# Optimization experiments

Measured on AMD Instinct MI355X. Metric: run time of the kernel, lower is better.

## Reference

```python
import jax, jax.numpy as jnp
import numpy as np

EMBED = 128; HEADS = 8; LEVELS = 3; POINTS = 4
SCENE = (128, 128, 8)
IMG_H, IMG_W = 370, 1226
VOXEL_SIZE = 0.4; OFFSET = 0.5
FEAT_SHAPES = ((47, 154), (24, 77), (12, 39))  # (H, W) per level, strides ~8/16/32
NVOX = SCENE[0] * SCENE[1] * SCENE[2]
DH = EMBED // HEADS


def layernorm(x, g, b, eps=1e-5):
    mu = x.mean(-1, keepdims=True)
    var = ((x - mu) ** 2).mean(-1, keepdims=True)
    return (x - mu) * jax.lax.rsqrt(var + eps) * g + b


def ms_deform(value, locs, aw):
    # value [B,Nv,H,Dh]; locs [B,Q,H,L,P,2] normalized (x,y); aw [B,Q,H,L,P]
    # Matches F.grid_sample(bilinear, zeros padding, align_corners=False):
    # pixel = loc * size - 0.5, per-corner gather with zeroed out-of-range weights.
    B, Nv, Hh, Dh = value.shape
    Q, P = locs.shape[1], locs.shape[4]
    out = jnp.zeros((B, Hh, Q, Dh), value.dtype)
    start = 0
    for l, (h, w) in enumerate(FEAT_SHAPES):
        v = value[:, start:start + h * w].transpose(0, 2, 1, 3)  # [B,H,h*w,Dh]
        start += h * w
        x = locs[:, :, :, l, :, 0] * w - 0.5  # [B,Q,H,P]
        y = locs[:, :, :, l, :, 1] * h - 0.5
        x0, y0 = jnp.floor(x), jnp.floor(y)
        a_l = aw[:, :, :, l]  # [B,Q,H,P]
        for dx in (0, 1):
            for dy in (0, 1):
                xi, yi = x0 + dx, y0 + dy
                wgt = (1.0 - jnp.abs(x - xi)) * (1.0 - jnp.abs(y - yi))
                valid = (xi >= 0) & (xi <= w - 1) & (yi >= 0) & (yi <= h - 1)
                coef = wgt * valid * a_l  # bilinear weight * attention weight
                idx = (jnp.clip(yi, 0, h - 1) * w + jnp.clip(xi, 0, w - 1)).astype(jnp.int32)
                idx = idx.transpose(0, 2, 1, 3).reshape(B, Hh, Q * P, 1)
                g = jnp.take_along_axis(v, idx, axis=2).reshape(B, Hh, Q, P, Dh)
                out = out + jnp.einsum('bhqpd,bqhp->bhqd', g, coef)
    return out.transpose(0, 2, 1, 3).reshape(B, Q, Hh * Dh)


def _forward(scene_embed, feat0, feat1, feat2, depth, K, E, voxel_origin, ref_pix,
             W_off, b_off, W_attn, b_attn, W_val, b_val, W_out, b_out,
             ln1_g, ln1_b, W_ffn1, b_ffn1, W_ffn2, b_ffn2, ln2_g, ln2_b):
    B = scene_embed.shape[0]
    # ---- camera-to-voxel projection (builds pts_mask) ----
    u = jnp.arange(IMG_W, dtype=jnp.float32)
    v = jnp.arange(IMG_H, dtype=jnp.float32)
    grid = jnp.stack([jnp.broadcast_to(u[None, :], (IMG_H, IMG_W)),
                      jnp.broadcast_to(v[:, None], (IMG_H, IMG_W))])[None]  # [1,2,H,W] (u,v)
    d = depth[:, None]  # [B,1,H,W]
    p_x = jnp.concatenate([grid * d, d], axis=1).reshape(B, 3, -1)  # homogeneous pixels
    p_c = jnp.linalg.inv(K) @ p_x  # camera frame [B,3,N]
    ones = jnp.ones((B, 1, p_c.shape[-1]), p_c.dtype)
    p_w = jnp.linalg.inv(E) @ jnp.concatenate([p_c, ones], axis=1)  # world frame [B,4,N]
    # torch .long() truncates toward zero -> jnp.trunc
    p_v = jnp.trunc((p_w[:, :3].transpose(0, 2, 1) - voxel_origin[:, None]) / VOXEL_SIZE - OFFSET).astype(jnp.int32)
    X, Y, Z = SCENE
    keep = ((p_v[..., 0] >= 0) & (p_v[..., 0] < X) &
            (p_v[..., 1] >= 0) & (p_v[..., 1] < Y) &
            (p_v[..., 2] >= 0) & (p_v[..., 2] < Z))
    lin = (p_v[..., 0] * Y + p_v[..., 1]) * Z + p_v[..., 2]
    lin = jnp.where(keep, lin, 0)
    pts_mask = (jnp.zeros((NVOX,), jnp.int32).at[lin[0]].max(keep[0].astype(jnp.int32)) > 0)

    # ---- MSDeformAttn layer over ALL voxel queries (per-query math is independent;
    #      masked selection + scatter-back is equivalent to a final where) ----
    feat_flat = jnp.concatenate(
        [f.reshape(B, EMBED, -1).transpose(0, 2, 1) for f in (feat0, feat1, feat2)], axis=1)
    value = (feat_flat @ W_val + b_val).reshape(B, -1, HEADS, DH)
    q = scene_embed  # [B,NVOX,C]
    off = (q @ W_off + b_off).reshape(B, NVOX, HEADS, LEVELS, POINTS, 2)
    aw = jax.nn.softmax((q @ W_attn + b_attn).reshape(B, NVOX, HEADS, LEVELS * POINTS), axis=-1)
    aw = aw.reshape(B, NVOX, HEADS, LEVELS, POINTS)
    norm = jnp.array([[w, h] for (h, w) in FEAT_SHAPES], jnp.float32)  # (W,H) per level
    locs = ref_pix[:, :, None, None, None, :] + off / norm[None, None, None, :, None, :]
    sampled = ms_deform(value, locs, aw)  # [B,NVOX,C]
    x = layernorm(sampled @ W_out + b_out + q, ln1_g, ln1_b)       # attn residual + norm1
    h = jax.nn.gelu(x @ W_ffn1 + b_ffn1, approximate=False)        # exact GELU (torch default)
    x = layernorm(h @ W_ffn2 + b_ffn2 + x, ln2_g, ln2_b)           # ffn residual + norm2

    # ---- index_fov_back_to_voxels: masked voxels get attn output, rest keep input ----
    return jnp.where(pts_mask[None, :, None], x, scene_embed)


def setup_inputs() -> dict:
    key = jax.random.key(0)
    ks = jax.random.split(key, 16)
    d = {}
    d['scene_embed'] = jax.random.normal(ks[0], (1, NVOX, EMBED), jnp.float32)
    for i, (h, w) in enumerate(FEAT_SHAPES):
        d[f'feat{i}'] = jax.random.normal(ks[1 + i], (1, EMBED, h, w), jnp.float32)
    d['depth'] = jax.random.uniform(ks[4], (1, IMG_H, IMG_W), jnp.float32) * 50.0 + 2.0
    d['K'] = jnp.array([[[707.0, 0.0, 602.0], [0.0, 707.0, 183.0], [0.0, 0.0, 1.0]]], jnp.float32)
    c, s = float(np.cos(0.02)), float(np.sin(0.02))
    d['E'] = jnp.array([[[c, -s, 0.0, 0.5], [s, c, 0.0, 0.1],
                         [0.0, 0.0, 1.0, -1.6], [0.0, 0.0, 0.0, 1.0]]], jnp.float32)
    d['voxel_origin'] = jnp.array([[0.0, -25.6, -2.0]], jnp.float32)
    d['ref_pix'] = jax.random.uniform(ks[5], (1, NVOX, 2), jnp.float32)

    def lin(k, fin, fout):
        s = 1.0 / float(np.sqrt(fin))
        kw, kb = jax.random.split(k)
        return (jax.random.uniform(kw, (fin, fout), jnp.float32, -s, s),
                jax.random.uniform(kb, (fout,), jnp.float32, -s, s))

    d['W_off'], d['b_off'] = lin(ks[6], EMBED, HEADS * LEVELS * POINTS * 2)
    d['W_attn'], d['b_attn'] = lin(ks[7], EMBED, HEADS * LEVELS * POINTS)
    d['W_val'], d['b_val'] = lin(ks[8], EMBED, EMBED)
    d['W_out'], d['b_out'] = lin(ks[9], EMBED, EMBED)
    d['ln1_g'] = jnp.ones((EMBED,), jnp.float32); d['ln1_b'] = jnp.zeros((EMBED,), jnp.float32)
    d['W_ffn1'], d['b_ffn1'] = lin(ks[10], EMBED, EMBED * 4)
    d['W_ffn2'], d['b_ffn2'] = lin(ks[11], EMBED * 4, EMBED)
    d['ln2_g'] = jnp.ones((EMBED,), jnp.float32); d['ln2_b'] = jnp.zeros((EMBED,), jnp.float32)
    return d


def reference(scene_embed, feat0, feat1, feat2, depth, K, E, voxel_origin, ref_pix,
              W_off, b_off, W_attn, b_attn, W_val, b_val, W_out, b_out,
              ln1_g, ln1_b, W_ffn1, b_ffn1, W_ffn2, b_ffn2, ln2_g, ln2_b):
    return _forward(scene_embed, feat0, feat1, feat2, depth, K, E, voxel_origin, ref_pix,
                    W_off, b_off, W_attn, b_attn, W_val, b_val, W_out, b_out,
                    ln1_g, ln1_b, W_ffn1, b_ffn1, W_ffn2, b_ffn2, ln2_g, ln2_b)
```

## Files before the change

kernel.cpp:

```cpp
#include <hip/hip_runtime.h>
#include <math.h>

#define NVOXT 131072
#define NPIX  (370*1226)
#define NVAL  9554
#define DMT   16

#define OFF_INV    0
#define OFF_CNT    256
#define OFF_MASK   512
#define OFF_LIST   (512 + 4*NVOXT)
#define OFF_VALUE  (OFF_LIST + 4*NVOXT)

__device__ void gauss_inv(const float* A, double* out, int n) {
    double a[4][8];
    for (int r = 0; r < n; r++)
        for (int c = 0; c < n; c++) {
            a[r][c]     = (double)A[r*n + c];
            a[r][n + c] = (r == c) ? 1.0 : 0.0;
        }
    for (int col = 0; col < n; col++) {
        int piv = col; double best = fabs(a[col][col]);
        for (int r = col + 1; r < n; r++) {
            double m = fabs(a[r][col]);
            if (m > best) { best = m; piv = r; }
        }
        if (piv != col)
            for (int c = 0; c < 2*n; c++) { double t = a[col][c]; a[col][c] = a[piv][c]; a[piv][c] = t; }
        double dinv = 1.0 / a[col][col];
        for (int c = 0; c < 2*n; c++) a[col][c] *= dinv;
        for (int r = 0; r < n; r++) if (r != col) {
            double f = a[r][col];
            for (int c = 0; c < 2*n; c++) a[r][c] -= f * a[col][c];
        }
    }
    for (int r = 0; r < n; r++)
        for (int c = 0; c < n; c++) out[r*n + c] = a[r][n + c];
}

__global__ void zero_kernel(int* mask, int* cnt, const float* Km, const float* Em,
                            double* inv) {
    int i = blockIdx.x * 256 + threadIdx.x;
    if (i < NVOXT) mask[i] = 0;
    if (i == 0) *cnt = 0;
    if (blockIdx.x == 512) {
        if (threadIdx.x == 0) gauss_inv(Km, inv, 3);
        if (threadIdx.x == 1) gauss_inv(Em, inv + 9, 4);
    }
}

__global__ void mask_kernel(const float* depth, const float* org,
                            const double* invd, int* mask) {
    __shared__ float iK[9], iE[12];
    if (threadIdx.x < 9)  iK[threadIdx.x] = (float)invd[threadIdx.x];
    if (threadIdx.x < 12) iE[threadIdx.x] = (float)invd[9 + threadIdx.x];
    __syncthreads();
    int i = blockIdx.x * 256 + threadIdx.x;
    if (i >= NPIX) return;
    int u = i % 1226, v = i / 1226;
    float d  = depth[i];
    float px = (float)u * d, py = (float)v * d, pz = d;
    float c0 = iK[0]*px + iK[1]*py + iK[2]*pz;
    float c1 = iK[3]*px + iK[4]*py + iK[5]*pz;
    float c2 = iK[6]*px + iK[7]*py + iK[8]*pz;
    float w0 = iE[0]*c0 + iE[1]*c1 + iE[2]*c2  + iE[3];
    float w1 = iE[4]*c0 + iE[5]*c1 + iE[6]*c2  + iE[7];
    float w2 = iE[8]*c0 + iE[9]*c1 + iE[10]*c2 + iE[11];
    float q0 = truncf((w0 - org[0]) / 0.4f - 0.5f);
    float q1 = truncf((w1 - org[1]) / 0.4f - 0.5f);
    float q2 = truncf((w2 - org[2]) / 0.4f - 0.5f);
    if (q0 >= 0.0f && q0 < 128.0f && q1 >= 0.0f && q1 < 128.0f && q2 >= 0.0f && q2 < 8.0f) {
        int lin = (((int)q0) * 128 + (int)q1) * 8 + (int)q2;
        atomicOr(&mask[lin], 1);
    }
}

__global__ void compact_kernel(const int* mask, int* list, int* cnt) {
    int v = blockIdx.x * 256 + threadIdx.x;
    if (v < NVOXT && mask[v]) {
        int p = atomicAdd(cnt, 1);
        list[p] = v;
    }
}

__global__ void copy_kernel(const float4* src, float4* dst) {
    int i = blockIdx.x * 256 + threadIdx.x;
    dst[i] = src[i];
}

__global__ __launch_bounds__(128) void value_kernel(
    const float* f0, const float* f1, const float* f2,
    const float* Wv, const float* bv, float* value) {
    __shared__ __align__(16) float As[16*129];
    int n0 = blockIdx.x * 16;
    int t  = threadIdx.x;
    for (int i = 0; i < 16; i++) {
        int flat = t + i*128;
        int k = flat >> 4, r = flat & 15;
        int n = n0 + r;
        float vload = 0.f;
        if (n < NVAL) {
            const float* f; int p, hw;
            if (n < 7238)      { f = f0; p = n;        hw = 7238; }
            else if (n < 9086) { f = f1; p = n - 7238; hw = 1848; }
            else               { f = f2; p = n - 9086; hw = 468;  }
            vload = f[k*hw + p];
        }
        As[r*129 + k] = vload;
    }
    __syncthreads();
    float acc[16];
    float bb = bv[t];
    #pragma unroll
    for (int r = 0; r < 16; r++) acc[r] = bb;
    for (int k = 0; k < 128; k++) {
        float w = Wv[k*128 + t];
        #pragma unroll
        for (int r = 0; r < 16; r++) acc[r] += As[r*129 + k] * w;
    }
    for (int r = 0; r < 16; r++) {
        int n = n0 + r;
        if (n < NVAL) value[n*128 + t] = acc[r];
    }
}

#define FMA4(A, s, Vv) { A[0] += (s)*(Vv).x; A[1] += (s)*(Vv).y; A[2] += (s)*(Vv).z; A[3] += (s)*(Vv).w; }

__global__ __launch_bounds__(256) void deform_kernel(
    const float* scene, const float* refpix,
    const float* Woff, const float* Wattn,
    const float* boff, const float* battn,
    const float* value, const float* Wout, const float* bout,
    const float* ln1g, const float* ln1b,
    const int* list, const int* cntp, float* out) {
    __shared__ __align__(16) float sQ[DMT*132];
    __shared__ __align__(16) float sW[9216];
    __shared__ __align__(16) float sOA[DMT*292];
    __shared__ __align__(16) float sSamp[DMT*132];

    const int count = *cntp;
    const int r0 = blockIdx.x * DMT;
    if (r0 >= count) return;
    const int t = threadIdx.x;

    for (int i = 0; i < 8; i++) {
        int flat = t + i*256;
        int m = flat >> 7, e = flat & 127;
        int r = r0 + m;
        float qv = 0.f;
        if (r < count) qv = scene[(size_t)list[r]*128 + e];
        sQ[m*132 + e] = qv;
    }
    __syncthreads();

    const int tn = t & 31, tm = t >> 5;
    float acc[3][2][4] = {};

    for (int c = 0; c < 4; c++) {
        __syncthreads();
        for (int i = 0; i < 24; i++) {
            int flat = t + i*256;
            int kk = flat / 192, n = flat % 192;
            sW[kk*288 + n] = Woff[(c*32 + kk)*192 + n];
        }
        for (int i = 0; i < 12; i++) {
            int flat = t + i*256;
            int kk = flat / 96, na = flat % 96;
            sW[kk*288 + 192 + na] = Wattn[(c*32 + kk)*96 + na];
        }
        __syncthreads();
        for (int kk = 0; kk < 32; kk++) {
            int k = c*32 + kk;
            float a0 = sQ[(2*tm)*132 + k];
            float a1 = sQ[(2*tm+1)*132 + k];
            float4 w0 = *(const float4*)&sW[kk*288 + 4*tn];
            float4 w1 = *(const float4*)&sW[kk*288 + 128 + 4*tn];
            FMA4(acc[0][0], a0, w0); FMA4(acc[0][1], a1, w0);
            FMA4(acc[1][0], a0, w1); FMA4(acc[1][1], a1, w1);
            if (tn < 8) {
                float4 w2 = *(const float4*)&sW[kk*288 + 256 + 4*tn];
                FMA4(acc[2][0], a0, w2); FMA4(acc[2][1], a1, w2);
            }
        }
    }
    for (int p = 0; p < 3; p++) {
        if (p == 2 && tn >= 8) continue;
        int nbase = p*128 + 4*tn;
        for (int i = 0; i < 2; i++)
            for (int j = 0; j < 4; j++) {
                int n = nbase + j;
                float bias = (n < 192) ? boff[n] : battn[n - 192];
                sOA[(2*tm+i)*292 + n] = acc[p][i][j] + bias;
            }
    }
    __syncthreads();

    {
        int v = t >> 4;
        int h = (t >> 1) & 7;
        int d0 = (t & 1) * 8;
        int r = r0 + v;
        int vox = (r < count) ? list[r] : list[0];
        float rx = refpix[vox*2 + 0], ry = refpix[vox*2 + 1];

        float L[12];
        float mx = -1e30f;
        #pragma unroll
        for (int j = 0; j < 12; j++) {
            L[j] = sOA[v*292 + 192 + h*12 + j];
            mx = fmaxf(mx, L[j]);
        }
        float s = 0.f;
        #pragma unroll
        for (int j = 0; j < 12; j++) { L[j] = expf(L[j] - mx); s += L[j]; }
        float inv_s = 1.f / s;

        const int   STl[3] = {0, 7238, 9086};
        const float FWl[3] = {154.f, 77.f, 39.f};
        const float FHl[3] = {47.f, 24.f, 12.f};

        float accA[4] = {0,0,0,0}, accB[4] = {0,0,0,0};
        for (int l = 0; l < 3; l++) {
            float fw = FWl[l], fh = FHl[l];
            int   st = STl[l];
            int   iw = (int)fw;
            for (int p = 0; p < 4; p++) {
                float ox = sOA[v*292 + h*24 + l*8 + p*2 + 0];
                float oy = sOA[v*292 + h*24 + l*8 + p*2 + 1];
                float x = rx*fw + ox - 0.5f;
                float y = ry*fh + oy - 0.5f;
                float aw = L[l*4 + p] * inv_s;
                float x0 = floorf(x), y0 = floorf(y);
                #pragma unroll
                for (int dy = 0; dy <= 1; dy++)
                #pragma unroll
                for (int dx = 0; dx <= 1; dx++) {
                    float xi = x0 + dx, yi = y0 + dy;
                    if (xi >= 0.f && xi <= fw - 1.f && yi >= 0.f && yi <= fh - 1.f) {
                        float cf = (1.f - fabsf(x - xi)) * (1.f - fabsf(y - yi)) * aw;
                        int idx = (int)yi * iw + (int)xi;
                        const float* vp = value + ((size_t)(st + idx)*128 + h*16 + d0);
                        float4 va = *(const float4*)vp;
                        float4 vb = *(const float4*)(vp + 4);
                        FMA4(accA, cf, va);
                        FMA4(accB, cf, vb);
                    }
                }
            }
        }
        float* sp = &sSamp[v*132 + h*16 + d0];
        *(float4*)sp       = make_float4(accA[0], accA[1], accA[2], accA[3]);
        *(float4*)(sp + 4) = make_float4(accB[0], accB[1], accB[2], accB[3]);
    }
    __syncthreads();

    float acc2[2][4] = {};
    for (int c = 0; c < 2; c++) {
        __syncthreads();
        for (int i = 0; i < 32; i++) {
            int flat = t + i*256;
            sW[flat] = Wout[c*8192 + flat];
        }
        __syncthreads();
        for (int kk = 0; kk < 64; kk++) {
            int k = c*64 + kk;
            float a0 = sSamp[(2*tm)*132 + k];
            float a1 = sSamp[(2*tm+1)*132 + k];
            float4 w = *(const float4*)&sW[kk*128 + 4*tn];
            FMA4(acc2[0], a0, w); FMA4(acc2[1], a1, w);
        }
    }
    __syncthreads();
    float* sX = sOA;
    for (int i = 0; i < 2; i++)
        for (int j = 0; j < 4; j++) {
            int n = 4*tn + j, m = 2*tm + i;
            sX[m*132 + n] = acc2[i][j] + bout[n] + sQ[m*132 + n];
        }
    __syncthreads();

    {
        int row = t >> 4, j16 = t & 15;
        float xs[8], s1 = 0.f, s2 = 0.f;
        #pragma unroll
        for (int q = 0; q < 8; q++) {
            float xv = sX[row*132 + j16*8 + q];
            xs[q] = xv; s1 += xv; s2 += xv*xv;
        }
        #pragma unroll
        for (int off = 8; off >= 1; off >>= 1) {
            s1 += __shfl_xor(s1, off, 16);
            s2 += __shfl_xor(s2, off, 16);
        }
        float mu  = s1 * (1.f/128.f);
        float var = s2 * (1.f/128.f) - mu*mu;
        float rs  = 1.f / sqrtf(var + 1e-5f);
        int r = r0 + row;
        if (r < count) {
            int vox = list[r];
            #pragma unroll
            for (int q = 0; q < 8; q++) {
                int e = j16*8 + q;
                out[(size_t)vox*128 + e] = (xs[q] - mu) * rs * ln1g[e] + ln1b[e];
            }
        }
    }
}

__global__ __launch_bounds__(256) void ffn_kernel(
    const float* W1, const float* b1,
    const float* W2, const float* b2,
    const float* ln2g, const float* ln2b,
    const int* list, const int* cntp, float* out) {
    __shared__ __align__(16) float sX[DMT*132];
    __shared__ __align__(16) float sW[8192];
    __shared__ __align__(16) float sH[DMT*516];

    const int count = *cntp;
    const int r0 = blockIdx.x * DMT;
    if (r0 >= count) return;
    const int t = threadIdx.x;

    for (int i = 0; i < 8; i++) {
        int flat = t + i*256;
        int m = flat >> 7, e = flat & 127;
        int r = r0 + m;
        sX[m*132 + e] = (r < count) ? out[(size_t)list[r]*128 + e] : 0.f;
    }
    const int tn = t & 31, tm = t >> 5;

    for (int pass = 0; pass < 4; pass++) {
        int n0 = pass * 128;
        float acc[2][4] = {};
        for (int c = 0; c < 2; c++) {
            __syncthreads();
            for (int i = 0; i < 32; i++) {
                int flat = t + i*256;
                int kk = flat >> 7, col = flat & 127;
                sW[flat] = W1[(c*64 + kk)*512 + n0 + col];
            }
            __syncthreads();
            for (int kk = 0; kk < 64; kk++) {
                int k = c*64 + kk;
                float a0 = sX[(2*tm)*132 + k];
                float a1 = sX[(2*tm+1)*132 + k];
                float4 w = *(const float4*)&sW[kk*128 + 4*tn];
                FMA4(acc[0], a0, w); FMA4(acc[1], a1, w);
            }
        }
        for (int i = 0; i < 2; i++)
            for (int j = 0; j < 4; j++) {
                int n = n0 + 4*tn + j;
                float hv = acc[i][j] + b1[n];
                float g  = 0.5f * hv * (1.f + erff(hv * 0.70710678118654752f));
                sH[(2*tm+i)*516 + n] = g;
            }
    }

    float acc2[2][4] = {};
    for (int c = 0; c < 8; c++) {
        __syncthreads();
        for (int i = 0; i < 32; i++) {
            int flat = t + i*256;
            sW[flat] = W2[c*8192 + flat];
        }
        __syncthreads();
        for (int kk = 0; kk < 64; kk++) {
            int k = c*64 + kk;
            float a0 = sH[(2*tm)*516 + k];
            float a1 = sH[(2*tm+1)*516 + k];
            float4 w = *(const float4*)&sW[kk*128 + 4*tn];
            FMA4(acc2[0], a0, w); FMA4(acc2[1], a1, w);
        }
    }
    __syncthreads();
    float* sY = sH;
    for (int i = 0; i < 2; i++)
        for (int j = 0; j < 4; j++) {
            int n = 4*tn + j, m = 2*tm + i;
            sY[m*132 + n] = acc2[i][j] + b2[n] + sX[m*132 + n];
        }
    __syncthreads();

    {
        int row = t >> 4, j16 = t & 15;
        float ys[8], s1 = 0.f, s2 = 0.f;
        #pragma unroll
        for (int q = 0; q < 8; q++) {
            float yv = sY[row*132 + j16*8 + q];
            ys[q] = yv; s1 += yv; s2 += yv*yv;
        }
        #pragma unroll
        for (int off = 8; off >= 1; off >>= 1) {
            s1 += __shfl_xor(s1, off, 16);
            s2 += __shfl_xor(s2, off, 16);
        }
        float mu  = s1 * (1.f/128.f);
        float var = s2 * (1.f/128.f) - mu*mu;
        float rs  = 1.f / sqrtf(var + 1e-5f);
        int r = r0 + row;
        if (r < count) {
            int vox = list[r];
            #pragma unroll
            for (int q = 0; q < 8; q++) {
                int e = j16*8 + q;
                out[(size_t)vox*128 + e] = (ys[q] - mu) * rs * ln2g[e] + ln2b[e];
            }
        }
    }
}

extern "C" void kernel_launch(void* const* d_in, const int* in_sizes, int n_in,
                              void* d_out, int out_size, void* d_ws, size_t ws_size,
                              hipStream_t stream) {
    const float* scene  = (const float*)d_in[0];
    const float* feat0  = (const float*)d_in[1];
    const float* feat1  = (const float*)d_in[2];
    const float* feat2  = (const float*)d_in[3];
    const float* depth  = (const float*)d_in[4];
    const float* Km     = (const float*)d_in[5];
    const float* Em     = (const float*)d_in[6];
    const float* vorg   = (const float*)d_in[7];
    const float* refpix = (const float*)d_in[8];
    const float* W_off  = (const float*)d_in[9];
    const float* b_off  = (const float*)d_in[10];
    const float* W_attn = (const float*)d_in[11];
    const float* b_attn = (const float*)d_in[12];
    const float* W_val  = (const float*)d_in[13];
    const float* b_val  = (const float*)d_in[14];
    const float* W_out  = (const float*)d_in[15];
    const float* b_out  = (const float*)d_in[16];
    const float* ln1g   = (const float*)d_in[17];
    const float* ln1b   = (const float*)d_in[18];
    const float* W_ffn1 = (const float*)d_in[19];
    const float* b_ffn1 = (const float*)d_in[20];
    const float* W_ffn2 = (const float*)d_in[21];
    const float* b_ffn2 = (const float*)d_in[22];
    const float* ln2g   = (const float*)d_in[23];
    const float* ln2b   = (const float*)d_in[24];

    char* ws = (char*)d_ws;
    double* inv   = (double*)(ws + OFF_INV);
    int*    cnt   = (int*)   (ws + OFF_CNT);
    int*    mask  = (int*)   (ws + OFF_MASK);
    int*    list  = (int*)   (ws + OFF_LIST);
    float*  value = (float*) (ws + OFF_VALUE);
    float*  outp  = (float*)d_out;

    zero_kernel<<<513, 256, 0, stream>>>(mask, cnt, Km, Em, inv);
    mask_kernel<<<1772, 256, 0, stream>>>(depth, vorg, inv, mask);
    compact_kernel<<<512, 256, 0, stream>>>(mask, list, cnt);
    value_kernel<<<598, 128, 0, stream>>>(feat0, feat1, feat2, W_val, b_val, value);
    copy_kernel<<<16384, 256, 0, stream>>>((const float4*)scene, (float4*)outp);
    deform_kernel<<<NVOXT/DMT, 256, 0, stream>>>(scene, refpix, W_off, W_attn,
                                                 b_off, b_attn, value,
                                                 W_out, b_out, ln1g, ln1b,
                                                 list, cnt, outp);
    ffn_kernel<<<NVOXT/DMT, 256, 0, stream>>>(W_ffn1, b_ffn1, W_ffn2, b_ffn2,
                                              ln2g, ln2b, list, cnt, outp);
}
```

Baseline: 201.5 us.

## Merge prologue kernels, fuse compaction into mask, use persistent grids

Zeroing, matrix inversion and the scene copy now run in one prologue kernel. Voxel-list compaction moves into the mask kernel: the first thread to set a voxel appends it, so the separate compaction pass disappears. The deform and FFN kernels switch from 8192 mostly-empty blocks to a 2048-block grid-stride loop, and the value kernel exits early when no voxels are found. This cuts launch count and idle-block overhead, but list order is now nondeterministic and each block processes rows serially.

```diff
diff --git a/kernel.cpp b/kernel.cpp
--- a/kernel.cpp
+++ b/kernel.cpp
@@ -38,19 +38,25 @@
         for (int c = 0; c < n; c++) out[r*n + c] = a[r][n + c];
 }
 
-__global__ void zero_kernel(int* mask, int* cnt, const float* Km, const float* Em,
-                            double* inv) {
-    int i = blockIdx.x * 256 + threadIdx.x;
-    if (i < NVOXT) mask[i] = 0;
-    if (i == 0) *cnt = 0;
-    if (blockIdx.x == 512) {
-        if (threadIdx.x == 0) gauss_inv(Km, inv, 3);
-        if (threadIdx.x == 1) gauss_inv(Em, inv + 9, 4);
+__global__ void prologue_kernel(const float* Km, const float* Em, double* inv,
+                                int* mask, int* cnt,
+                                const float4* src, float4* dst) {
+    int bid = blockIdx.x;
+    if (bid < 512) {
+        mask[bid*256 + threadIdx.x] = 0;
+        if (bid == 0) {
+            if (threadIdx.x == 64) *cnt = 0;
+            if (threadIdx.x == 0) gauss_inv(Km, inv, 3);
+            if (threadIdx.x == 1) gauss_inv(Em, inv + 9, 4);
+        }
+    } else {
+        int i = (bid - 512)*256 + threadIdx.x;
+        dst[i] = src[i];
     }
 }
 
 __global__ void mask_kernel(const float* depth, const float* org,
-                            const double* invd, int* mask) {
+                            const double* invd, int* mask, int* list, int* cnt) {
     __shared__ float iK[9], iE[12];
     if (threadIdx.x < 9)  iK[threadIdx.x] = (float)invd[threadIdx.x];
     if (threadIdx.x < 12) iE[threadIdx.x] = (float)invd[9 + threadIdx.x];
@@ -71,26 +77,17 @@
     float q2 = truncf((w2 - org[2]) / 0.4f - 0.5f);
     if (q0 >= 0.0f && q0 < 128.0f && q1 >= 0.0f && q1 < 128.0f && q2 >= 0.0f && q2 < 8.0f) {
         int lin = (((int)q0) * 128 + (int)q1) * 8 + (int)q2;
-        atomicOr(&mask[lin], 1);
-    }
-}
-
-__global__ void compact_kernel(const int* mask, int* list, int* cnt) {
-    int v = blockIdx.x * 256 + threadIdx.x;
-    if (v < NVOXT && mask[v]) {
-        int p = atomicAdd(cnt, 1);
-        list[p] = v;
-    }
-}
-
-__global__ void copy_kernel(const float4* src, float4* dst) {
-    int i = blockIdx.x * 256 + threadIdx.x;
-    dst[i] = src[i];
+        if (atomicOr(&mask[lin], 1) == 0) {
+            int p = atomicAdd(cnt, 1);
+            list[p] = lin;
+        }
+    }
 }
 
 __global__ __launch_bounds__(128) void value_kernel(
     const float* f0, const float* f1, const float* f2,
-    const float* Wv, const float* bv, float* value) {
+    const float* Wv, const float* bv, const int* cntp, float* value) {
+    if (*cntp == 0) return;
     __shared__ __align__(16) float As[16*129];
     int n0 = blockIdx.x * 16;
     int t  = threadIdx.x;
@@ -139,9 +136,10 @@
     __shared__ __align__(16) float sSamp[DMT*132];
 
     const int count = *cntp;
-    const int r0 = blockIdx.x * DMT;
-    if (r0 >= count) return;
     const int t = threadIdx.x;
+    const int tn = t & 31, tm = t >> 5;
+
+    for (int r0 = blockIdx.x * DMT; r0 < count; r0 += gridDim.x * DMT) {
 
     for (int i = 0; i < 8; i++) {
         int flat = t + i*256;
@@ -153,7 +151,6 @@
     }
     __syncthreads();
 
-    const int tn = t & 31, tm = t >> 5;
     float acc[3][2][4] = {};
 
     for (int c = 0; c < 4; c++) {
@@ -305,6 +302,8 @@
             }
         }
     }
+
+    }
 }
 
 __global__ __launch_bounds__(256) void ffn_kernel(
@@ -317,9 +316,10 @@
     __shared__ __align__(16) float sH[DMT*516];
 
     const int count = *cntp;
-    const int r0 = blockIdx.x * DMT;
-    if (r0 >= count) return;
     const int t = threadIdx.x;
+    const int tn = t & 31, tm = t >> 5;
+
+    for (int r0 = blockIdx.x * DMT; r0 < count; r0 += gridDim.x * DMT) {
 
     for (int i = 0; i < 8; i++) {
         int flat = t + i*256;
@@ -327,7 +327,6 @@
         int r = r0 + m;
         sX[m*132 + e] = (r < count) ? out[(size_t)list[r]*128 + e] : 0.f;
     }
-    const int tn = t & 31, tm = t >> 5;
 
     for (int pass = 0; pass < 4; pass++) {
         int n0 = pass * 128;
@@ -407,6 +406,8 @@
                 out[(size_t)vox*128 + e] = (ys[q] - mu) * rs * ln2g[e] + ln2b[e];
             }
         }
+    }
+
     }
 }
 
@@ -447,15 +448,15 @@
     float*  value = (float*) (ws + OFF_VALUE);
     float*  outp  = (float*)d_out;
 
-    zero_kernel<<<513, 256, 0, stream>>>(mask, cnt, Km, Em, inv);
-    mask_kernel<<<1772, 256, 0, stream>>>(depth, vorg, inv, mask);
-    compact_kernel<<<512, 256, 0, stream>>>(mask, list, cnt);
-    value_kernel<<<598, 128, 0, stream>>>(feat0, feat1, feat2, W_val, b_val, value);
-    copy_kernel<<<16384, 256, 0, stream>>>((const float4*)scene, (float4*)outp);
-    deform_kernel<<<NVOXT/DMT, 256, 0, stream>>>(scene, refpix, W_off, W_attn,
-                                                 b_off, b_attn, value,
-                                                 W_out, b_out, ln1g, ln1b,
-                                                 list, cnt, outp);
-    ffn_kernel<<<NVOXT/DMT, 256, 0, stream>>>(W_ffn1, b_ffn1, W_ffn2, b_ffn2,
-                                              ln2g, ln2b, list, cnt, outp);
-}
+    prologue_kernel<<<16896, 256, 0, stream>>>(Km, Em, inv, mask, cnt,
+                                               (const float4*)scene, (float4*)outp);
+    mask_kernel<<<1772, 256, 0, stream>>>(depth, vorg, inv, mask, list, cnt);
+    value_kernel<<<598, 128, 0, stream>>>(feat0, feat1, feat2, W_val, b_val,
+                                          cnt, value);
+    deform_kernel<<<2048, 256, 0, stream>>>(scene, refpix, W_off, W_attn,
+                                            b_off, b_attn, value,
+                                            W_out, b_out, ln1g, ln1b,
+                                            list, cnt, outp);
+    ffn_kernel<<<2048, 256, 0, stream>>>(W_ffn1, b_ffn1, W_ffn2, b_ffn2,
+                                         ln2g, ln2b, list, cnt, outp);
+}
```

Result: faster. 167.7 us (-16.8%).
